# Kernel tuning notes

Hardware: AMD Instinct MI355X
Metric: run time of the kernel (lower is better)

Reference implementation:

```python
import jax, jax.numpy as jnp
import numpy as np

NEG_SLOPE = 0.2
EPS = 1e-16


def setup_inputs() -> dict:
    key = jax.random.key(0)
    k1, k2, k3, k4 = jax.random.split(key, 4)
    N, H, F, E = 50000, 4, 32, 800000
    nodes_features = jax.random.normal(k1, (N, H, F), dtype=jnp.float32)
    edge_index = jax.random.randint(k2, (2, E), 0, N, dtype=jnp.int64)
    scoring_fn_source = jax.random.normal(k3, (1, H, F), dtype=jnp.float32)
    scoring_fn_target = jax.random.normal(k4, (1, H, F), dtype=jnp.float32)
    return {
        "nodes_features": nodes_features,
        "scoring_fn_source": scoring_fn_source,
        "scoring_fn_target": scoring_fn_target,
        "edge_index": edge_index,
    }


def reference(nodes_features, scoring_fn_source, scoring_fn_target, edge_index):
    # nodes_features: [N, H, F]; edge_index: [2, E] with row 0 = target, row 1 = source
    num_of_nodes = nodes_features.shape[0]
    trg = edge_index[0]
    src = edge_index[1]

    # Per-node attention logits per head: [N, H]
    scores_source = (nodes_features * scoring_fn_source).sum(axis=-1)
    scores_target = (nodes_features * scoring_fn_target).sum(axis=-1)

    # Lift N -> E via gather: [E, H]
    scores_lifted = scores_source[src] + scores_target[trg]
    src_nodes_features_lifted = nodes_features[src]  # [E, H, F]

    scores_per_edge = jax.nn.leaky_relu(scores_lifted, NEG_SLOPE)
    # Global max subtraction for numerical stability (matches original code)
    scores_per_edge = scores_per_edge - scores_per_edge.max()
    exp_scores = jnp.exp(scores_per_edge)

    # Segment softmax denominator via scatter-add, then gather back per edge
    neighborhood_sums = jax.ops.segment_sum(exp_scores, trg, num_segments=num_of_nodes)
    denom = neighborhood_sums[trg]  # [E, H]

    attentions_per_edge = (exp_scores / (denom + EPS))[..., None]  # [E, H, 1]
    return attentions_per_edge, src_nodes_features_lifted
```

## Files before the change

### kernel.cpp

```cpp
#include <hip/hip_runtime.h>
#include <hip/hip_bf16.h>

#define NEG_SLOPE 0.2f
#define EPSV 1e-16f

typedef float f32x4 __attribute__((ext_vector_type(4)));
typedef float f32x2 __attribute__((ext_vector_type(2)));
typedef short s16x2 __attribute__((ext_vector_type(2)));
typedef unsigned u32x2 __attribute__((ext_vector_type(2)));

__device__ __forceinline__ unsigned fenc(float f) {
    unsigned b = __float_as_uint(f);
    return b ^ ((b & 0x80000000u) ? 0xFFFFFFFFu : 0x80000000u);
}
__device__ __forceinline__ float fdec(unsigned u) {
    unsigned b = (u & 0x80000000u) ? (u ^ 0x80000000u) : ~u;
    return __uint_as_float(b);
}
#define FENC_NEG_INF 0x007FFFFFu

__device__ __forceinline__ unsigned f32_to_bf16_rne(float f) {
    unsigned u = __float_as_uint(f);
    unsigned lsb = (u >> 16) & 1u;
    return (u + 0x7FFFu + lsb) >> 16;
}

__device__ __forceinline__ void pk_atomic_add_bf16(unsigned* addr, float a, float b) {
#if __has_builtin(__builtin_amdgcn_global_atomic_fadd_v2bf16)
    s16x2 v;
    v.x = (short)f32_to_bf16_rne(a);
    v.y = (short)f32_to_bf16_rne(b);
    typedef __attribute__((address_space(1))) s16x2 gs16x2;
    __builtin_amdgcn_global_atomic_fadd_v2bf16((gs16x2*)(void*)addr, v);
#else
    unsigned old = *addr, assumed;
    do {
        assumed = old;
        float lo = __uint_as_float((assumed & 0xFFFFu) << 16) + a;
        float hi = __uint_as_float(assumed & 0xFFFF0000u) + b;
        unsigned nv = (f32_to_bf16_rne(hi) << 16) | (f32_to_bf16_rne(lo) & 0xFFFFu);
        old = atomicCAS(addr, assumed, nv);
    } while (old != assumed);
#endif
}

__global__ void detect_idx_kernel(const unsigned* __restrict__ ei32,
                                  int* __restrict__ flag) {
    __shared__ int anynz;
    if (threadIdx.x == 0) anynz = 0;
    __syncthreads();
    unsigned v = ei32[2 * threadIdx.x + 1];
    if (v != 0u) anynz = 1;
    __syncthreads();
    if (threadIdx.x == 0) *flag = (anynz ? 0 : 1);
}

__device__ __forceinline__ int load_idx(const void* ei, int is64, size_t k) {
    if (is64) return (int)__builtin_nontemporal_load(&((const long long*)ei)[k]);
    return __builtin_nontemporal_load(&((const int*)ei)[k]);
}

__global__ void node_scores_kernel(const float* __restrict__ nf,
                                   const float* __restrict__ sfs,
                                   const float* __restrict__ sft,
                                   float* __restrict__ ss,
                                   float* __restrict__ st,
                                   unsigned* __restrict__ nsum_zero,
                                   unsigned* __restrict__ gmax,
                                   int NH, int nzero) {
    int i = blockIdx.x * blockDim.x + threadIdx.x;
    if (i >= NH) return;
    if (i == 0) *gmax = FENC_NEG_INF;
    for (int k = i; k < nzero; k += NH) nsum_zero[k] = 0u;
    int h = i & 3;
    const float4* __restrict__ row = (const float4*)(nf + (size_t)i * 32);
    const float4* __restrict__ as  = (const float4*)(sfs + h * 32);
    const float4* __restrict__ at  = (const float4*)(sft + h * 32);
    float accs = 0.f, acct = 0.f;
#pragma unroll
    for (int q = 0; q < 8; ++q) {
        float4 v = row[q];
        float4 a = as[q];
        float4 b = at[q];
        accs += v.x * a.x + v.y * a.y + v.z * a.z + v.w * a.w;
        acct += v.x * b.x + v.y * b.y + v.z * b.z + v.w * b.w;
    }
    ss[i] = accs;
    st[i] = acct;
}

__global__ void edge_exp_sum_pk_kernel(const void* __restrict__ ei,
                                       const int* __restrict__ flag,
                                       const float* __restrict__ ss,
                                       const float* __restrict__ st,
                                       float* __restrict__ pbuf,
                                       unsigned* __restrict__ nsum_pk,
                                       unsigned* __restrict__ gmax,
                                       int E) {
    __shared__ float red[256];
    int is64 = *flag;
    int n2 = E * 2;
    int stride = gridDim.x * blockDim.x;
    float lmax = -__builtin_inff();
    for (int i = blockIdx.x * blockDim.x + threadIdx.x; i < n2; i += stride) {
        int e = i >> 1, hp = i & 1;
        int trg = load_idx(ei, is64, e);
        int src = load_idx(ei, is64, (size_t)E + e);
        f32x2 a = *(const f32x2*)(ss + (size_t)src * 4 + hp * 2);
        f32x2 b = *(const f32x2*)(st + (size_t)trg * 4 + hp * 2);
        float s0 = a.x + b.x, s1 = a.y + b.y;
        float lr0 = s0 > 0.f ? s0 : NEG_SLOPE * s0;
        float lr1 = s1 > 0.f ? s1 : NEG_SLOPE * s1;
        lmax = fmaxf(lmax, fmaxf(lr0, lr1));
        float p0 = __expf(lr0), p1 = __expf(lr1);
        f32x2 pv; pv.x = p0; pv.y = p1;
        __builtin_nontemporal_store(pv, (f32x2*)(pbuf + (size_t)e * 4 + hp * 2));
        pk_atomic_add_bf16(nsum_pk + (size_t)trg * 2 + hp, p0, p1);
    }
    red[threadIdx.x] = lmax;
    __syncthreads();
    for (int off = 128; off > 0; off >>= 1) {
        if (threadIdx.x < off)
            red[threadIdx.x] = fmaxf(red[threadIdx.x], red[threadIdx.x + off]);
        __syncthreads();
    }
    if (threadIdx.x == 0) atomicMax(gmax, fenc(red[0]));
}

__global__ void att_pk_kernel(const void* __restrict__ ei,
                              const int* __restrict__ flag,
                              const float* __restrict__ pbuf,
                              const unsigned* __restrict__ nsum_pk,
                              const unsigned* __restrict__ gmax,
                              float* __restrict__ out,
                              int E) {
    int is64 = *flag;
    float de = EPSV * __expf(fdec(*gmax));
    int stride = gridDim.x * blockDim.x;
    for (int e = blockIdx.x * blockDim.x + threadIdx.x; e < E; e += stride) {
        int trg = load_idx(ei, is64, e);
        u32x2 u = *(const u32x2*)(nsum_pk + (size_t)trg * 2);
        f32x4 d;
        d.x = __uint_as_float((u.x & 0xFFFFu) << 16);
        d.y = __uint_as_float(u.x & 0xFFFF0000u);
        d.z = __uint_as_float((u.y & 0xFFFFu) << 16);
        d.w = __uint_as_float(u.y & 0xFFFF0000u);
        f32x4 p = __builtin_nontemporal_load((const f32x4*)(pbuf + (size_t)e * 4));
        f32x4 a = p / (d + de);
        __builtin_nontemporal_store(a, (f32x4*)(out + (size_t)e * 4));
    }
}

__global__ void gather_feat_kernel(const void* __restrict__ ei,
                                   const int* __restrict__ flag,
                                   const f32x4* __restrict__ nf4,
                                   f32x4* __restrict__ out4, int E) {
    int is64 = *flag;
    int n = E * 32;
    int stride = gridDim.x * blockDim.x;
    for (int t = blockIdx.x * blockDim.x + threadIdx.x; t < n; t += stride) {
        int e = t >> 5, q = t & 31;
        int src = load_idx(ei, is64, (size_t)E + e);
        f32x4 v = nf4[(size_t)src * 32 + q];
        __builtin_nontemporal_store(v, &out4[(size_t)e * 32 + q]);
    }
}

__device__ __forceinline__ float edge_lr_rc(const void* ei, int is64,
                                            const float* ss, const float* st,
                                            int E, int e, int h, int* trg_out) {
    int trg = load_idx(ei, is64, e);
    int src = load_idx(ei, is64, (size_t)E + e);
    if (trg_out) *trg_out = trg;
    float s = ss[src * 4 + h] + st[trg * 4 + h];
    return s > 0.f ? s : NEG_SLOPE * s;
}

__global__ void zero_fb_kernel(float* __restrict__ nsum, int n) {
    int i = blockIdx.x * blockDim.x + threadIdx.x;
    if (i < n) nsum[i] = 0.f;
}

__global__ void edge_exp_sum_fb_kernel(const void* __restrict__ ei,
                                       const int* __restrict__ flag,
                                       const float* __restrict__ ss,
                                       const float* __restrict__ st,
                                       float* __restrict__ nsum,
                                       unsigned* __restrict__ gmax, int E) {
    __shared__ float red[256];
    int is64 = *flag;
    int n4 = E * 4;
    int stride = gridDim.x * blockDim.x;
    float lmax = -__builtin_inff();
    for (int i = blockIdx.x * blockDim.x + threadIdx.x; i < n4; i += stride) {
        int trg;
        float lr = edge_lr_rc(ei, is64, ss, st, E, i >> 2, i & 3, &trg);
        lmax = fmaxf(lmax, lr);
        atomicAdd(&nsum[trg * 4 + (i & 3)], __expf(lr));
    }
    red[threadIdx.x] = lmax;
    __syncthreads();
    for (int off = 128; off > 0; off >>= 1) {
        if (threadIdx.x < off)
            red[threadIdx.x] = fmaxf(red[threadIdx.x], red[threadIdx.x + off]);
        __syncthreads();
    }
    if (threadIdx.x == 0) atomicMax(gmax, fenc(red[0]));
}

__global__ void att_fb_kernel(const void* __restrict__ ei,
                              const int* __restrict__ flag,
                              const float* __restrict__ ss,
                              const float* __restrict__ st,
                              const unsigned* __restrict__ gmax,
                              const float* __restrict__ nsum,
                              float* __restrict__ out, int E) {
    int i = blockIdx.x * blockDim.x + threadIdx.x;
    if (i >= E * 4) return;
    int is64 = *flag;
    float de = EPSV * __expf(fdec(*gmax));
    int trg;
    float lr = edge_lr_rc(ei, is64, ss, st, E, i >> 2, i & 3, &trg);
    float a = __expf(lr) / (nsum[trg * 4 + (i & 3)] + de);
    __builtin_nontemporal_store(a, &out[i]);
}

extern "C" void kernel_launch(void* const* d_in, const int* in_sizes, int n_in,
                              void* d_out, int out_size, void* d_ws, size_t ws_size,
                              hipStream_t stream) {
    const float* nf  = (const float*)d_in[0];
    const float* sfs = (const float*)d_in[1];
    const float* sft = (const float*)d_in[2];
    const void*  ei  = d_in[3];

    const int NH = in_sizes[0] / 32;
    const int N  = NH / 4;
    const int E  = in_sizes[3] / 2;

    float* out = (float*)d_out;
    float* ws  = (float*)d_ws;

    float*    ss      = ws;
    float*    st      = ws + NH;
    int*      flag    = (int*)(ws + 2 * (size_t)NH);
    unsigned* gmax    = (unsigned*)(flag + 1);
    float*    pbuf    = ws + 2 * (size_t)NH + 4;
    unsigned* nsum_pk = (unsigned*)(pbuf + (size_t)E * 4);

    size_t need = ((size_t)2 * NH + 4 + (size_t)E * 4 + (size_t)N * 2) * 4;
    bool lean = ws_size >= need;

    const int B = 256;

    detect_idx_kernel<<<1, 256, 0, stream>>>((const unsigned*)ei, flag);

    if (lean) {
        node_scores_kernel<<<(NH + B - 1) / B, B, 0, stream>>>(
            nf, sfs, sft, ss, st, nsum_pk, gmax, NH, N * 2);
        edge_exp_sum_pk_kernel<<<2048, B, 0, stream>>>(ei, flag, ss, st, pbuf,
                                                       nsum_pk, gmax, E);
        att_pk_kernel<<<2048, B, 0, stream>>>(ei, flag, pbuf, nsum_pk, gmax,
                                              out, E);
        gather_feat_kernel<<<4096, B, 0, stream>>>(
            ei, flag, (const f32x4*)nf, (f32x4*)(out + (size_t)E * 4), E);
    } else {
        float* nsum_fb = (float*)(gmax + 1);
        node_scores_kernel<<<(NH + B - 1) / B, B, 0, stream>>>(
            nf, sfs, sft, ss, st, (unsigned*)nsum_fb, gmax, NH, 0);
        zero_fb_kernel<<<(NH + B - 1) / B, B, 0, stream>>>(nsum_fb, NH);
        edge_exp_sum_fb_kernel<<<2048, B, 0, stream>>>(ei, flag, ss, st,
                                                       nsum_fb, gmax, E);
        att_fb_kernel<<<(E * 4 + B - 1) / B, B, 0, stream>>>(ei, flag, ss, st,
                                                             gmax, nsum_fb, out, E);
        gather_feat_kernel<<<4096, B, 0, stream>>>(
            ei, flag, (const f32x4*)nf, (f32x4*)(out + (size_t)E * 4), E);
    }
}
```

Baseline: 237.5 us.

## Fuse edge exp-sum and attention kernels via cooperative grid sync, keep exps in registers

Merges the exp/scatter-sum kernel and the normalization kernel into one cooperative kernel that synchronizes the whole grid after the global max and neighbor sums are ready. Each thread keeps up to eight exp values and target indices in registers, which removes the per-edge pbuf round trip through global memory and one launch. Threads with more than eight items recompute their scores instead. The feature gather kernel also now copies two float4 per thread instead of one. The grid shrinks to 1024 blocks to fit cooperative residency, which may reduce memory-level parallelism, and the dynamic register indexing may add register pressure.

```diff
diff --git a/kernel.cpp b/kernel.cpp
--- a/kernel.cpp
+++ b/kernel.cpp
@@ -1,8 +1,10 @@
 #include <hip/hip_runtime.h>
-#include <hip/hip_bf16.h>
+#include <hip/hip_cooperative_groups.h>
 
 #define NEG_SLOPE 0.2f
 #define EPSV 1e-16f
+
+namespace cg = cooperative_groups;
 
 typedef float f32x4 __attribute__((ext_vector_type(4)));
 typedef float f32x2 __attribute__((ext_vector_type(2)));
@@ -89,20 +91,27 @@
     st[i] = acct;
 }
 
-__global__ void edge_exp_sum_pk_kernel(const void* __restrict__ ei,
-                                       const int* __restrict__ flag,
-                                       const float* __restrict__ ss,
-                                       const float* __restrict__ st,
-                                       float* __restrict__ pbuf,
-                                       unsigned* __restrict__ nsum_pk,
-                                       unsigned* __restrict__ gmax,
-                                       int E) {
+#define MAXI 8
+__global__ void fused_edge_kernel(const void* __restrict__ ei,
+                                  const int* __restrict__ flag,
+                                  const float* __restrict__ ss,
+                                  const float* __restrict__ st,
+                                  unsigned* __restrict__ nsum_pk,
+                                  unsigned* __restrict__ gmax,
+                                  float* __restrict__ out,
+                                  int E) {
     __shared__ float red[256];
     int is64 = *flag;
     int n2 = E * 2;
     int stride = gridDim.x * blockDim.x;
+    int base = blockIdx.x * blockDim.x + threadIdx.x;
+
+    f32x2 preg[MAXI];
+    int   treg[MAXI];
     float lmax = -__builtin_inff();
-    for (int i = blockIdx.x * blockDim.x + threadIdx.x; i < n2; i += stride) {
+
+    int it = 0;
+    for (int i = base; i < n2; i += stride, ++it) {
         int e = i >> 1, hp = i & 1;
         int trg = load_idx(ei, is64, e);
         int src = load_idx(ei, is64, (size_t)E + e);
@@ -113,10 +122,15 @@
         float lr1 = s1 > 0.f ? s1 : NEG_SLOPE * s1;
         lmax = fmaxf(lmax, fmaxf(lr0, lr1));
         float p0 = __expf(lr0), p1 = __expf(lr1);
-        f32x2 pv; pv.x = p0; pv.y = p1;
-        __builtin_nontemporal_store(pv, (f32x2*)(pbuf + (size_t)e * 4 + hp * 2));
+        if (it < MAXI) {
+            f32x2 pv; pv.x = p0; pv.y = p1;
+#pragma unroll
+            for (int k = 0; k < MAXI; ++k)
+                if (k == it) { preg[k] = pv; treg[k] = trg; }
+        }
         pk_atomic_add_bf16(nsum_pk + (size_t)trg * 2 + hp, p0, p1);
     }
+
     red[threadIdx.x] = lmax;
     __syncthreads();
     for (int off = 128; off > 0; off >>= 1) {
@@ -125,29 +139,35 @@
         __syncthreads();
     }
     if (threadIdx.x == 0) atomicMax(gmax, fenc(red[0]));
-}
-
-__global__ void att_pk_kernel(const void* __restrict__ ei,
-                              const int* __restrict__ flag,
-                              const float* __restrict__ pbuf,
-                              const unsigned* __restrict__ nsum_pk,
-                              const unsigned* __restrict__ gmax,
-                              float* __restrict__ out,
-                              int E) {
-    int is64 = *flag;
+
+    cg::this_grid().sync();
+
     float de = EPSV * __expf(fdec(*gmax));
-    int stride = gridDim.x * blockDim.x;
-    for (int e = blockIdx.x * blockDim.x + threadIdx.x; e < E; e += stride) {
-        int trg = load_idx(ei, is64, e);
-        u32x2 u = *(const u32x2*)(nsum_pk + (size_t)trg * 2);
-        f32x4 d;
-        d.x = __uint_as_float((u.x & 0xFFFFu) << 16);
-        d.y = __uint_as_float(u.x & 0xFFFF0000u);
-        d.z = __uint_as_float((u.y & 0xFFFFu) << 16);
-        d.w = __uint_as_float(u.y & 0xFFFF0000u);
-        f32x4 p = __builtin_nontemporal_load((const f32x4*)(pbuf + (size_t)e * 4));
-        f32x4 a = p / (d + de);
-        __builtin_nontemporal_store(a, (f32x4*)(out + (size_t)e * 4));
+    it = 0;
+    for (int i = base; i < n2; i += stride, ++it) {
+        int e = i >> 1, hp = i & 1;
+        f32x2 pv;
+        int trg;
+        if (it < MAXI) {
+#pragma unroll
+            for (int k = 0; k < MAXI; ++k)
+                if (k == it) { pv = preg[k]; trg = treg[k]; }
+        } else {
+            trg = load_idx(ei, is64, e);
+            int src = load_idx(ei, is64, (size_t)E + e);
+            f32x2 a = *(const f32x2*)(ss + (size_t)src * 4 + hp * 2);
+            f32x2 b = *(const f32x2*)(st + (size_t)trg * 4 + hp * 2);
+            float s0 = a.x + b.x, s1 = a.y + b.y;
+            float lr0 = s0 > 0.f ? s0 : NEG_SLOPE * s0;
+            float lr1 = s1 > 0.f ? s1 : NEG_SLOPE * s1;
+            pv.x = __expf(lr0); pv.y = __expf(lr1);
+        }
+        unsigned u = nsum_pk[(size_t)trg * 2 + hp];
+        f32x2 d;
+        d.x = __uint_as_float((u & 0xFFFFu) << 16);
+        d.y = __uint_as_float(u & 0xFFFF0000u);
+        f32x2 a = pv / (d + de);
+        __builtin_nontemporal_store(a, (f32x2*)(out + (size_t)e * 4 + hp * 2));
     }
 }
 
@@ -156,13 +176,17 @@
                                    const f32x4* __restrict__ nf4,
                                    f32x4* __restrict__ out4, int E) {
     int is64 = *flag;
-    int n = E * 32;
+    int n = E * 16;
     int stride = gridDim.x * blockDim.x;
     for (int t = blockIdx.x * blockDim.x + threadIdx.x; t < n; t += stride) {
-        int e = t >> 5, q = t & 31;
+        int e = t >> 4, q = (t & 15) * 2;
         int src = load_idx(ei, is64, (size_t)E + e);
-        f32x4 v = nf4[(size_t)src * 32 + q];
-        __builtin_nontemporal_store(v, &out4[(size_t)e * 32 + q]);
+        const f32x4* sp = nf4 + (size_t)src * 32 + q;
+        f32x4 v0 = sp[0];
+        f32x4 v1 = sp[1];
+        f32x4* dp = out4 + (size_t)e * 32 + q;
+        __builtin_nontemporal_store(v0, dp);
+        __builtin_nontemporal_store(v1, dp + 1);
     }
 }
 
@@ -244,10 +268,9 @@
     float*    st      = ws + NH;
     int*      flag    = (int*)(ws + 2 * (size_t)NH);
     unsigned* gmax    = (unsigned*)(flag + 1);
-    float*    pbuf    = ws + 2 * (size_t)NH + 4;
-    unsigned* nsum_pk = (unsigned*)(pbuf + (size_t)E * 4);
-
-    size_t need = ((size_t)2 * NH + 4 + (size_t)E * 4 + (size_t)N * 2) * 4;
+    unsigned* nsum_pk = (unsigned*)(ws + 2 * (size_t)NH + 4);
+
+    size_t need = ((size_t)2 * NH + 4 + (size_t)N * 2) * 4;
     bool lean = ws_size >= need;
 
     const int B = 256;
@@ -257,10 +280,12 @@
     if (lean) {
         node_scores_kernel<<<(NH + B - 1) / B, B, 0, stream>>>(
             nf, sfs, sft, ss, st, nsum_pk, gmax, NH, N * 2);
-        edge_exp_sum_pk_kernel<<<2048, B, 0, stream>>>(ei, flag, ss, st, pbuf,
-                                                       nsum_pk, gmax, E);
-        att_pk_kernel<<<2048, B, 0, stream>>>(ei, flag, pbuf, nsum_pk, gmax,
-                                              out, E);
+
+        void* args[] = {(void*)&ei, (void*)&flag, (void*)&ss, (void*)&st,
+                        (void*)&nsum_pk, (void*)&gmax, (void*)&out, (void*)&E};
+        hipLaunchCooperativeKernel((const void*)fused_edge_kernel,
+                                   dim3(1024), dim3(B), args, 0, stream);
+
         gather_feat_kernel<<<4096, B, 0, stream>>>(
             ei, flag, (const f32x4*)nf, (f32x4*)(out + (size_t)E * 4), E);
     } else {
```

Result: slower. 377.8 us (+59.1%).

## Recompute edge exponentials instead of buffering; precompute per-node reciprocal denominators

Applied to the files above, without the earlier changes.

The per-edge exp buffer written by the sum kernel and read back by the attention kernel is removed. The attention kernel now regathers node scores by source and target, recomputes the leaky-relu and exp, and multiplies by a per-node reciprocal denominator built by a new small kernel. This drops a 12.8 MB write and read of intermediate data and replaces a division with a multiply. In exchange it adds a kernel launch and extra random gathers of ss, st and rinv for every edge and head, with one thread per edge-head instead of vectorized float4 handling.

```diff
diff --git a/kernel.cpp b/kernel.cpp
--- a/kernel.cpp
+++ b/kernel.cpp
@@ -1,5 +1,4 @@
 #include <hip/hip_runtime.h>
-#include <hip/hip_bf16.h>
 
 #define NEG_SLOPE 0.2f
 #define EPSV 1e-16f
@@ -7,7 +6,6 @@
 typedef float f32x4 __attribute__((ext_vector_type(4)));
 typedef float f32x2 __attribute__((ext_vector_type(2)));
 typedef short s16x2 __attribute__((ext_vector_type(2)));
-typedef unsigned u32x2 __attribute__((ext_vector_type(2)));
 
 __device__ __forceinline__ unsigned fenc(float f) {
     unsigned b = __float_as_uint(f);
@@ -93,7 +91,6 @@
                                        const int* __restrict__ flag,
                                        const float* __restrict__ ss,
                                        const float* __restrict__ st,
-                                       float* __restrict__ pbuf,
                                        unsigned* __restrict__ nsum_pk,
                                        unsigned* __restrict__ gmax,
                                        int E) {
@@ -113,8 +110,6 @@
         float lr1 = s1 > 0.f ? s1 : NEG_SLOPE * s1;
         lmax = fmaxf(lmax, fmaxf(lr0, lr1));
         float p0 = __expf(lr0), p1 = __expf(lr1);
-        f32x2 pv; pv.x = p0; pv.y = p1;
-        __builtin_nontemporal_store(pv, (f32x2*)(pbuf + (size_t)e * 4 + hp * 2));
         pk_atomic_add_bf16(nsum_pk + (size_t)trg * 2 + hp, p0, p1);
     }
     red[threadIdx.x] = lmax;
@@ -127,27 +122,37 @@
     if (threadIdx.x == 0) atomicMax(gmax, fenc(red[0]));
 }
 
-__global__ void att_pk_kernel(const void* __restrict__ ei,
+__global__ void rinv_kernel(const unsigned* __restrict__ nsum_pk,
+                            const unsigned* __restrict__ gmax,
+                            float* __restrict__ rinv,
+                            int NH) {
+    int i = blockIdx.x * blockDim.x + threadIdx.x;
+    if (i >= NH) return;
+    float de = EPSV * __expf(fdec(*gmax));
+    unsigned u = nsum_pk[i >> 1];
+    float d = (i & 1) ? __uint_as_float(u & 0xFFFF0000u)
+                      : __uint_as_float((u & 0xFFFFu) << 16);
+    rinv[i] = 1.f / (d + de);
+}
+
+__global__ void att_rc_kernel(const void* __restrict__ ei,
                               const int* __restrict__ flag,
-                              const float* __restrict__ pbuf,
-                              const unsigned* __restrict__ nsum_pk,
-                              const unsigned* __restrict__ gmax,
+                              const float* __restrict__ ss,
+                              const float* __restrict__ st,
+                              const float* __restrict__ rinv,
                               float* __restrict__ out,
                               int E) {
     int is64 = *flag;
-    float de = EPSV * __expf(fdec(*gmax));
-    int stride = gridDim.x * blockDim.x;
-    for (int e = blockIdx.x * blockDim.x + threadIdx.x; e < E; e += stride) {
+    int n4 = E * 4;
+    int stride = gridDim.x * blockDim.x;
+    for (int i = blockIdx.x * blockDim.x + threadIdx.x; i < n4; i += stride) {
+        int e = i >> 2, h = i & 3;
         int trg = load_idx(ei, is64, e);
-        u32x2 u = *(const u32x2*)(nsum_pk + (size_t)trg * 2);
-        f32x4 d;
-        d.x = __uint_as_float((u.x & 0xFFFFu) << 16);
-        d.y = __uint_as_float(u.x & 0xFFFF0000u);
-        d.z = __uint_as_float((u.y & 0xFFFFu) << 16);
-        d.w = __uint_as_float(u.y & 0xFFFF0000u);
-        f32x4 p = __builtin_nontemporal_load((const f32x4*)(pbuf + (size_t)e * 4));
-        f32x4 a = p / (d + de);
-        __builtin_nontemporal_store(a, (f32x4*)(out + (size_t)e * 4));
+        int src = load_idx(ei, is64, (size_t)E + e);
+        float s = ss[src * 4 + h] + st[trg * 4 + h];
+        float lr = s > 0.f ? s : NEG_SLOPE * s;
+        float a = __expf(lr) * rinv[trg * 4 + h];
+        __builtin_nontemporal_store(a, &out[i]);
     }
 }
 
@@ -244,10 +249,10 @@
     float*    st      = ws + NH;
     int*      flag    = (int*)(ws + 2 * (size_t)NH);
     unsigned* gmax    = (unsigned*)(flag + 1);
-    float*    pbuf    = ws + 2 * (size_t)NH + 4;
-    unsigned* nsum_pk = (unsigned*)(pbuf + (size_t)E * 4);
-
-    size_t need = ((size_t)2 * NH + 4 + (size_t)E * 4 + (size_t)N * 2) * 4;
+    unsigned* nsum_pk = (unsigned*)(ws + 2 * (size_t)NH + 4);
+    float*    rinv    = (float*)(nsum_pk + (size_t)N * 2);
+
+    size_t need = ((size_t)3 * NH + 4 + (size_t)N * 2) * 4;
     bool lean = ws_size >= need;
 
     const int B = 256;
@@ -257,10 +262,10 @@
     if (lean) {
         node_scores_kernel<<<(NH + B - 1) / B, B, 0, stream>>>(
             nf, sfs, sft, ss, st, nsum_pk, gmax, NH, N * 2);
-        edge_exp_sum_pk_kernel<<<2048, B, 0, stream>>>(ei, flag, ss, st, pbuf,
+        edge_exp_sum_pk_kernel<<<2048, B, 0, stream>>>(ei, flag, ss, st,
                                                        nsum_pk, gmax, E);
-        att_pk_kernel<<<2048, B, 0, stream>>>(ei, flag, pbuf, nsum_pk, gmax,
-                                              out, E);
+        rinv_kernel<<<(NH + B - 1) / B, B, 0, stream>>>(nsum_pk, gmax, rinv, NH);
+        att_rc_kernel<<<4096, B, 0, stream>>>(ei, flag, ss, st, rinv, out, E);
         gather_feat_kernel<<<4096, B, 0, stream>>>(
             ei, flag, (const f32x4*)nf, (f32x4*)(out + (size_t)E * 4), E);
     } else {
```

New measurement: 245.5 us. +3.4%, slower.

## Bin edges by source node and gather features per XCD-local bin

Applied to the files above, without the earlier changes.

Adds a counting sort of edges into bins of 256 source nodes (histogram, serial scan, scatter producing a permutation and sorted source list). The feature gather then walks bins, assigning each bin to one XCD via blockIdx&7, so each XCD's L2 holds only the source rows of its own bins. The aim is to raise cache hit rates on the 409 MB output gather, whose random reads of the 25.6 MB node table otherwise spread across all XCD L2s. The cost is three extra kernels, extra workspace for perm and ssrc, and scattered writes to the output. The sort path only runs if the workspace is large enough.

```diff
diff --git a/kernel.cpp b/kernel.cpp
--- a/kernel.cpp
+++ b/kernel.cpp
@@ -1,8 +1,9 @@
 #include <hip/hip_runtime.h>
-#include <hip/hip_bf16.h>
 
 #define NEG_SLOPE 0.2f
 #define EPSV 1e-16f
+#define NBMAX 256
+#define BSHIFT 8
 
 typedef float f32x4 __attribute__((ext_vector_type(4)));
 typedef float f32x2 __attribute__((ext_vector_type(2)));
@@ -45,12 +46,14 @@
 }
 
 __global__ void detect_idx_kernel(const unsigned* __restrict__ ei32,
-                                  int* __restrict__ flag) {
+                                  int* __restrict__ flag,
+                                  unsigned* __restrict__ bhist) {
     __shared__ int anynz;
     if (threadIdx.x == 0) anynz = 0;
     __syncthreads();
     unsigned v = ei32[2 * threadIdx.x + 1];
     if (v != 0u) anynz = 1;
+    if (threadIdx.x < NBMAX) bhist[threadIdx.x] = 0u;
     __syncthreads();
     if (threadIdx.x == 0) *flag = (anynz ? 0 : 1);
 }
@@ -89,6 +92,68 @@
     st[i] = acct;
 }
 
+__global__ void bin_hist_kernel(const void* __restrict__ ei,
+                                const int* __restrict__ flag,
+                                unsigned* __restrict__ bhist, int E) {
+    __shared__ unsigned lh[NBMAX];
+    for (int i = threadIdx.x; i < NBMAX; i += blockDim.x) lh[i] = 0u;
+    __syncthreads();
+    int is64 = *flag;
+    int per = (E + gridDim.x - 1) / gridDim.x;
+    int s = blockIdx.x * per;
+    int en = s + per < E ? s + per : E;
+    for (int e = s + threadIdx.x; e < en; e += blockDim.x) {
+        int src = load_idx(ei, is64, (size_t)E + e);
+        atomicAdd(&lh[src >> BSHIFT], 1u);
+    }
+    __syncthreads();
+    for (int i = threadIdx.x; i < NBMAX; i += blockDim.x)
+        if (lh[i]) atomicAdd(&bhist[i], lh[i]);
+}
+
+__global__ void bin_scan_kernel(const unsigned* __restrict__ bhist,
+                                unsigned* __restrict__ bstart,
+                                unsigned* __restrict__ bcursor, int nb) {
+    if (threadIdx.x == 0) {
+        unsigned acc = 0;
+        for (int c = 0; c < nb; ++c) {
+            bstart[c] = acc;
+            bcursor[c] = acc;
+            acc += bhist[c];
+        }
+        bstart[nb] = acc;
+    }
+}
+
+__global__ void bin_scatter_kernel(const void* __restrict__ ei,
+                                   const int* __restrict__ flag,
+                                   unsigned* __restrict__ bcursor,
+                                   int* __restrict__ perm,
+                                   int* __restrict__ ssrc, int E) {
+    __shared__ unsigned lh[NBMAX], lbase[NBMAX], lcur[NBMAX];
+    for (int i = threadIdx.x; i < NBMAX; i += blockDim.x) { lh[i] = 0u; lcur[i] = 0u; }
+    __syncthreads();
+    int is64 = *flag;
+    int per = (E + gridDim.x - 1) / gridDim.x;
+    int s = blockIdx.x * per;
+    int en = s + per < E ? s + per : E;
+    for (int e = s + threadIdx.x; e < en; e += blockDim.x) {
+        int src = load_idx(ei, is64, (size_t)E + e);
+        atomicAdd(&lh[src >> BSHIFT], 1u);
+    }
+    __syncthreads();
+    for (int i = threadIdx.x; i < NBMAX; i += blockDim.x)
+        lbase[i] = lh[i] ? atomicAdd(&bcursor[i], lh[i]) : 0u;
+    __syncthreads();
+    for (int e = s + threadIdx.x; e < en; e += blockDim.x) {
+        int src = load_idx(ei, is64, (size_t)E + e);
+        int b = src >> BSHIFT;
+        unsigned pos = lbase[b] + atomicAdd(&lcur[b], 1u);
+        perm[pos] = e;
+        ssrc[pos] = src;
+    }
+}
+
 __global__ void edge_exp_sum_pk_kernel(const void* __restrict__ ei,
                                        const int* __restrict__ flag,
                                        const float* __restrict__ ss,
@@ -151,6 +216,27 @@
     }
 }
 
+__global__ void gather_sorted_kernel(const unsigned* __restrict__ bstart,
+                                     const int* __restrict__ perm,
+                                     const int* __restrict__ ssrc,
+                                     const f32x4* __restrict__ nf4,
+                                     f32x4* __restrict__ out4, int nb) {
+    int xcd = blockIdx.x & 7;
+    int lb = blockIdx.x >> 3;
+    int lstride = (gridDim.x >> 3) * blockDim.x;
+    for (int c = xcd; c < nb; c += 8) {
+        int js = (int)bstart[c];
+        int n = ((int)bstart[c + 1] - js) << 5;
+        for (int t = lb * blockDim.x + threadIdx.x; t < n; t += lstride) {
+            int j = js + (t >> 5), q = t & 31;
+            int e = perm[j];
+            int src = ssrc[j];
+            f32x4 v = nf4[(size_t)src * 32 + q];
+            __builtin_nontemporal_store(v, &out4[(size_t)e * 32 + q]);
+        }
+    }
+}
+
 __global__ void gather_feat_kernel(const void* __restrict__ ei,
                                    const int* __restrict__ flag,
                                    const f32x4* __restrict__ nf4,
@@ -236,6 +322,7 @@
     const int NH = in_sizes[0] / 32;
     const int N  = NH / 4;
     const int E  = in_sizes[3] / 2;
+    const int nb = (N + (1 << BSHIFT) - 1) >> BSHIFT;
 
     float* out = (float*)d_out;
     float* ws  = (float*)d_ws;
@@ -246,23 +333,41 @@
     unsigned* gmax    = (unsigned*)(flag + 1);
     float*    pbuf    = ws + 2 * (size_t)NH + 4;
     unsigned* nsum_pk = (unsigned*)(pbuf + (size_t)E * 4);
-
-    size_t need = ((size_t)2 * NH + 4 + (size_t)E * 4 + (size_t)N * 2) * 4;
-    bool lean = ws_size >= need;
+    unsigned* bhist   = nsum_pk + (size_t)N * 2;
+    unsigned* bstart  = bhist + NBMAX;
+    unsigned* bcursor = bstart + NBMAX + 1;
+    int*      perm    = (int*)(bcursor + NBMAX);
+    int*      ssrc    = perm + E;
+
+    size_t need_r9   = ((size_t)2 * NH + 4 + (size_t)E * 4 + (size_t)N * 2) * 4;
+    size_t need_sort = need_r9 + ((size_t)3 * NBMAX + 1 + (size_t)E * 2) * 4;
+    bool lean = ws_size >= need_r9;
+    bool srt  = ws_size >= need_sort;
 
     const int B = 256;
 
-    detect_idx_kernel<<<1, 256, 0, stream>>>((const unsigned*)ei, flag);
+    detect_idx_kernel<<<1, 256, 0, stream>>>((const unsigned*)ei, flag, bhist);
 
     if (lean) {
         node_scores_kernel<<<(NH + B - 1) / B, B, 0, stream>>>(
             nf, sfs, sft, ss, st, nsum_pk, gmax, NH, N * 2);
+        if (srt) {
+            bin_hist_kernel<<<256, B, 0, stream>>>(ei, flag, bhist, E);
+            bin_scan_kernel<<<1, 64, 0, stream>>>(bhist, bstart, bcursor, nb);
+            bin_scatter_kernel<<<256, B, 0, stream>>>(ei, flag, bcursor, perm, ssrc, E);
+        }
         edge_exp_sum_pk_kernel<<<2048, B, 0, stream>>>(ei, flag, ss, st, pbuf,
                                                        nsum_pk, gmax, E);
         att_pk_kernel<<<2048, B, 0, stream>>>(ei, flag, pbuf, nsum_pk, gmax,
                                               out, E);
-        gather_feat_kernel<<<4096, B, 0, stream>>>(
-            ei, flag, (const f32x4*)nf, (f32x4*)(out + (size_t)E * 4), E);
+        if (srt) {
+            gather_sorted_kernel<<<4096, B, 0, stream>>>(
+                bstart, perm, ssrc, (const f32x4*)nf,
+                (f32x4*)(out + (size_t)E * 4), nb);
+        } else {
+            gather_feat_kernel<<<4096, B, 0, stream>>>(
+                ei, flag, (const f32x4*)nf, (f32x4*)(out + (size_t)E * 4), E);
+        }
     } else {
         float* nsum_fb = (float*)(gmax + 1);
         node_scores_kernel<<<(NH + B - 1) / B, B, 0, stream>>>(
```

Result: faster. 219.9 us (median of 2 runs) (-7.4%).
